# Kernel optimization log

Measured on AMD Instinct MI355X. Metric: run time of the kernel, lower is better.

Reference implementation:

```python
import jax, jax.numpy as jnp
import numpy as np

HEADS = 8
MODEL_DIM = 64
EPS = 1e-5


def _layernorm(x, gamma, beta):
    mu = jnp.mean(x, axis=-1, keepdims=True)
    var = jnp.var(x, axis=-1, keepdims=True)
    return (x - mu) * jax.lax.rsqrt(var + EPS) * gamma + beta


def setup_inputs() -> dict:
    key = jax.random.key(0)
    ks = jax.random.split(key, 5)
    bs, h, w, in_dim = 8, 32, 32, 512
    hd = HEADS * MODEL_DIM  # 512
    s = 0.02
    return {
        "x": jax.random.normal(ks[0], (bs, h, w, in_dim), jnp.float32),
        "Wq": jax.random.normal(ks[1], (in_dim, hd), jnp.float32) * s,
        "Wk": jax.random.normal(ks[2], (in_dim, hd), jnp.float32) * s,
        "Wv": jax.random.normal(ks[3], (in_dim, hd), jnp.float32) * s,
        "Wo": jax.random.normal(ks[4], (hd, in_dim), jnp.float32) * s,
        "gamma": jnp.ones((in_dim,), jnp.float32),
        "beta": jnp.zeros((in_dim,), jnp.float32),
    }


def reference(x, Wq, Wk, Wv, Wo, gamma, beta):
    bs, h, w, in_dim = x.shape
    # pre_norm=True: normalize first; residual uses the normalized x (as in original)
    xn = _layernorm(x, gamma, beta)
    Q = (xn @ Wq).reshape(bs, h, w, HEADS, MODEL_DIM)
    K = (xn @ Wk).reshape(bs, h, w, HEADS, MODEL_DIM)
    V = (xn @ Wv).reshape(bs, h, w, HEADS, MODEL_DIM)
    # full (h,w) x (h,w) correlation per head
    corr = jnp.einsum('bijhd,bklhd->bijhkl', Q, K) / jnp.sqrt(
        jnp.asarray(MODEL_DIM, x.dtype))
    cshape = corr.shape
    attn = jax.nn.softmax(corr.reshape(*cshape[:-2], -1), axis=-1).reshape(cshape)
    logits = jnp.einsum('bijhkl,bklhd->bijhd', attn, V).reshape(bs, h, w, -1)
    out = logits @ Wo + xn
    return out, attn
```

## Files before the change

### kernel.cpp

```cpp
#include <hip/hip_runtime.h>
#include <hip/hip_bf16.h>

typedef __attribute__((ext_vector_type(8))) short bf16x8;
typedef __attribute__((ext_vector_type(4))) short s16x4;
typedef __attribute__((ext_vector_type(4))) float f32x4;

#define DIM 512
#define NH 8
#define HD 64
#define SEQ 1024
#define NB 8
#define ROWS (NB*SEQ)

__device__ __forceinline__ short f2bf(float f) {
  union { float f; unsigned u; } v; v.f = f;
  unsigned r = v.u + 0x7fffu + ((v.u >> 16) & 1u);
  return (short)(r >> 16);
}
__device__ __forceinline__ float bf2f(short s) {
  union { unsigned u; float f; } v; v.u = ((unsigned)(unsigned short)s) << 16;
  return v.f;
}
__device__ __forceinline__ f32x4 mfma16(bf16x8 a, bf16x8 b, f32x4 c) {
  return __builtin_amdgcn_mfma_f32_16x16x32_bf16(a, b, c, 0, 0, 0);
}
__device__ __forceinline__ void gload16(const void* g, void* l) {
  __builtin_amdgcn_global_load_lds(
      (const __attribute__((address_space(1))) unsigned int*)g,
      (__attribute__((address_space(3))) unsigned int*)l, 16, 0, 0);
}
__device__ __forceinline__ void lds_barrier() {
  __builtin_amdgcn_sched_barrier(0);
  asm volatile("s_waitcnt lgkmcnt(0)" ::: "memory");
  __builtin_amdgcn_s_barrier();
  __builtin_amdgcn_sched_barrier(0);
}

__global__ __launch_bounds__(256) void prep_kernel(
    const float* __restrict__ x, const float* __restrict__ gamma,
    const float* __restrict__ beta, short* __restrict__ xnb,
    const float* __restrict__ Wq, const float* __restrict__ Wk,
    const float* __restrict__ Wv, const float* __restrict__ Wo,
    short* __restrict__ WqkvT, short* __restrict__ WoT) {
  __shared__ float tl[64 * 65];
  const int t = threadIdx.x;
  if (blockIdx.x < 2048) {
    const int row = blockIdx.x * 4 + (t >> 6);
    const int lane = t & 63;
    const float4* xr = reinterpret_cast<const float4*>(x + (size_t)row * DIM);
    const float4 a = xr[lane * 2], b2 = xr[lane * 2 + 1];
    float s = a.x + a.y + a.z + a.w + b2.x + b2.y + b2.z + b2.w;
    float sq = a.x*a.x + a.y*a.y + a.z*a.z + a.w*a.w +
               b2.x*b2.x + b2.y*b2.y + b2.z*b2.z + b2.w*b2.w;
    for (int off = 1; off < 64; off <<= 1) {
      s += __shfl_xor(s, off);
      sq += __shfl_xor(sq, off);
    }
    const float mean = s * (1.0f / DIM);
    const float var = sq * (1.0f / DIM) - mean * mean;
    const float rs = rsqrtf(var + 1e-5f);
    const float4 ga = reinterpret_cast<const float4*>(gamma)[lane * 2];
    const float4 gb = reinterpret_cast<const float4*>(gamma)[lane * 2 + 1];
    const float4 ba = reinterpret_cast<const float4*>(beta)[lane * 2];
    const float4 bb = reinterpret_cast<const float4*>(beta)[lane * 2 + 1];
    union { bf16x8 v; short sh[8]; } o;
    o.sh[0] = f2bf((a.x - mean) * rs * ga.x + ba.x);
    o.sh[1] = f2bf((a.y - mean) * rs * ga.y + ba.y);
    o.sh[2] = f2bf((a.z - mean) * rs * ga.z + ba.z);
    o.sh[3] = f2bf((a.w - mean) * rs * ga.w + ba.w);
    o.sh[4] = f2bf((b2.x - mean) * rs * gb.x + bb.x);
    o.sh[5] = f2bf((b2.y - mean) * rs * gb.y + bb.y);
    o.sh[6] = f2bf((b2.z - mean) * rs * gb.z + bb.z);
    o.sh[7] = f2bf((b2.w - mean) * rs * gb.w + bb.w);
    *reinterpret_cast<bf16x8*>(xnb + (size_t)row * DIM + lane * 8) = o.v;
  } else {
    const int bb = blockIdx.x - 2048;
    const int y = bb >> 6;
    const float* W = (y == 0) ? Wq : (y == 1) ? Wk : (y == 2) ? Wv : Wo;
    const int tile = bb & 63;
    const int k0 = (tile >> 3) * 64, n0 = (tile & 7) * 64;
#pragma unroll
    for (int i = 0; i < 16; ++i) {
      const int idx = i * 256 + t;
      const int k = idx >> 6, n = idx & 63;
      tl[n * 65 + k] = W[(size_t)(k0 + k) * 512 + n0 + n];
    }
    __syncthreads();
#pragma unroll
    for (int i = 0; i < 16; ++i) {
      const int idx = i * 256 + t;
      const int n = idx >> 6, k = idx & 63;
      const short v = f2bf(tl[n * 65 + k]);
      if (y < 3) WqkvT[(size_t)(y * 512 + n0 + n) * 512 + k0 + k] = v;
      else       WoT[(size_t)(n0 + n) * 512 + k0 + k] = v;
    }
  }
}

#define GEMM64_MAIN(A_, BT_, m0_, n0_)                                        \
  f32x4 acc[4][4] = {};                                                       \
  {                                                                           \
    const int srow = 8 * w + (lane >> 3);                                     \
    const int sseg = lane & 7;                                                \
    for (int kb = 0; kb < 512; kb += 64) {                                    \
      __syncthreads();                                                        \
      _Pragma("unroll")                                                       \
      for (int p = 0; p < 4; ++p) {                                           \
        const int r = 32 * p + srow;                                          \
        const int gs = 8 * (sseg ^ (r & 7));                                  \
        gload16(A_ + (size_t)(m0_ + r) * 512 + kb + gs,                       \
                &As[(32 * p + 8 * w) * 64]);                                  \
        gload16(BT_ + (size_t)(n0_ + r) * 512 + kb + gs,                      \
                &Bs[(32 * p + 8 * w) * 64]);                                  \
      }                                                                       \
      __syncthreads();                                                        \
      _Pragma("unroll")                                                       \
      for (int half = 0; half < 2; ++half) {                                  \
        bf16x8 af[4], bfr[4];                                                 \
        _Pragma("unroll")                                                     \
        for (int i = 0; i < 4; ++i) {                                         \
          const int ra = 64 * wr + 16 * i + c16;                              \
          af[i] = *reinterpret_cast<const bf16x8*>(                           \
              &As[ra * 64 + 8 * ((4 * half + g) ^ (ra & 7))]);                \
          const int rb = 64 * wc + 16 * i + c16;                              \
          bfr[i] = *reinterpret_cast<const bf16x8*>(                          \
              &Bs[rb * 64 + 8 * ((4 * half + g) ^ (rb & 7))]);                \
        }                                                                     \
        _Pragma("unroll")                                                     \
        for (int i = 0; i < 4; ++i)                                           \
          _Pragma("unroll")                                                   \
          for (int j = 0; j < 4; ++j)                                         \
            acc[i][j] = mfma16(af[i], bfr[j], acc[i][j]);                     \
      }                                                                       \
    }                                                                         \
  }

__global__ __launch_bounds__(256) void gemm_qkv(const short* __restrict__ A,
    const short* __restrict__ BT, short* __restrict__ Qo,
    short* __restrict__ Ko, short* __restrict__ VtF) {
  __shared__ short As[128 * 64];
  __shared__ short Bs[128 * 64];
  const int m0 = blockIdx.x * 128, n0 = blockIdx.y * 128;
  const int t = threadIdx.x, w = t >> 6, lane = t & 63, g = lane >> 4, c16 = lane & 15;
  const int wr = w >> 1, wc = w & 1;
  GEMM64_MAIN(A, BT, m0, n0)
  const int z = n0 >> 9;
  const int nl = n0 & 511;
  if (z < 2) {
    short* O = (z == 0) ? Qo : Ko;
#pragma unroll
    for (int i = 0; i < 4; ++i)
#pragma unroll
      for (int j = 0; j < 4; ++j) {
        const int row0 = m0 + 64 * wr + 16 * i + 4 * g;
        const int col = nl + 64 * wc + 16 * j + c16;
#pragma unroll
        for (int e = 0; e < 4; ++e)
          O[(size_t)(row0 + e) * 512 + col] = f2bf(acc[i][j][e]);
      }
  } else {
#pragma unroll
    for (int i = 0; i < 4; ++i)
#pragma unroll
      for (int j = 0; j < 4; ++j) {
        const int row0 = m0 + 64 * wr + 16 * i + 4 * g;
        const int col = nl + 64 * wc + 16 * j + c16;
        const int bb = row0 >> 10, ss0 = row0 & 1023, hh = col >> 6, dd = col & 63;
        const int cch = ss0 >> 7, kk = ss0 & 127;
        const int w2 = kk >> 5;
        const int g2 = (kk >> 2) & 3;
        const int ee0 = 4 * ((kk >> 4) & 1) + (kk & 3);
        const int dt2 = dd >> 4, c162 = dd & 15;
        s16x4 pv;
#pragma unroll
        for (int e = 0; e < 4; ++e) pv[e] = f2bf(acc[i][j][e]);
        *reinterpret_cast<s16x4*>(
            &VtF[((size_t)((((bb * NH + hh) * 8 + cch) * 4 + w2) * 4 + dt2) << 9) +
                 (g2 * 16 + c162) * 8 + ee0]) = pv;
      }
  }
}

__global__ __launch_bounds__(256) void gemm_out(const short* __restrict__ A,
    const short* __restrict__ BT, const short* __restrict__ xnb,
    float* __restrict__ out) {
  __shared__ short As[128 * 64];
  __shared__ short Bs[128 * 64];
  const int m0 = blockIdx.x * 128, n0 = blockIdx.y * 128;
  const int t = threadIdx.x, w = t >> 6, lane = t & 63, g = lane >> 4, c16 = lane & 15;
  const int wr = w >> 1, wc = w & 1;
  GEMM64_MAIN(A, BT, m0, n0)
#pragma unroll
  for (int i = 0; i < 4; ++i)
#pragma unroll
    for (int j = 0; j < 4; ++j)
#pragma unroll
      for (int e = 0; e < 4; ++e) {
        const int row = m0 + 64 * wr + 16 * i + 4 * g + e;
        const int col = n0 + 64 * wc + 16 * j + c16;
        const size_t idx = (size_t)row * 512 + col;
        out[idx] = acc[i][j][e] + bf2f(xnb[idx]);
      }
}

__global__ __launch_bounds__(256, 2) void attn_kernel(
    const short* __restrict__ Qb, const short* __restrict__ Kb,
    const short* __restrict__ VtF, float* __restrict__ attnOut,
    short* __restrict__ Lg) {
  const int bid = blockIdx.x;
  const int rb = (bid >> 3) & 15;
  const int inst = (bid & 7) * 8 + (bid >> 7);
  const int b = inst >> 3, h = inst & 7;
  const int t = threadIdx.x;
  const int w = t >> 6, lane = t & 63, g = lane >> 4, c16 = lane & 15;
  const int rl = lane >> 3, sgl = lane & 7;
  const int sw = c16 & 7;
  const int rbase = rb * 64;
  const int qrow = t >> 4, qs = t & 15;

  __shared__ __align__(16) char smem[49664];
  __shared__ float red[2][4][16];
  short* Klds = (short*)smem;
  float* P32a = (float*)(smem + 32768);
  float* P32b = (float*)(smem + 41216);

  const short* kgbase = Kb + ((size_t)b * SEQ) * DIM + h * HD;
  const short* vf = VtF + (size_t)inst * 65536;
  const int swz = 8 * (sgl ^ rl);

#define KSTAGE(c_, buf_)                                                       \
  do {                                                                         \
    __builtin_amdgcn_sched_barrier(0);                                         \
    _Pragma("unroll") for (int i_ = 0; i_ < 4; ++i_) {                         \
      gload16(kgbase + (size_t)((c_) * 128 + 32 * w + 8 * i_ + rl) * DIM + swz,\
              &Klds[(buf_) * 8192 + (32 * w + 8 * i_) * 64]);                  \
    }                                                                          \
  } while (0)

  f32x4 acc[16] = {};
  {
    const short* qp = Qb + ((size_t)(b * SEQ + rbase + c16)) * DIM + h * HD + 8 * g;
    const bf16x8 q0 = *reinterpret_cast<const bf16x8*>(qp);
    const bf16x8 q1 = *reinterpret_cast<const bf16x8*>(qp + 32);
    KSTAGE(0, 0);
#pragma unroll
    for (int c = 0; c < 8; ++c) {
      if (c < 7) KSTAGE(c + 1, (c + 1) & 1);
      if (c < 7) { asm volatile("s_waitcnt vmcnt(4)" ::: "memory"); }
      else       { asm volatile("s_waitcnt vmcnt(0)" ::: "memory"); }
      __builtin_amdgcn_sched_barrier(0);
      const short* kl = &Klds[(c & 1) * 8192];
#pragma unroll
      for (int j = 0; j < 2; ++j) {
        const int lr = 32 * w + 16 * j + c16;
        bf16x8 k0 = *reinterpret_cast<const bf16x8*>(&kl[lr * 64 + 8 * (g ^ sw)]);
        bf16x8 k1 = *reinterpret_cast<const bf16x8*>(&kl[lr * 64 + 8 * ((g + 4) ^ sw)]);
        const int tt = c * 2 + j;
        acc[tt] = mfma16(k0, q0, acc[tt]);
        acc[tt] = mfma16(k1, q1, acc[tt]);
      }
    }
  }

  bf16x8 kreg[4], vreg[4];
#pragma unroll
  for (int i = 0; i < 4; ++i)
    kreg[i] = *reinterpret_cast<const bf16x8*>(
        kgbase + (size_t)(32 * w + 8 * i + rl) * DIM + 8 * sgl);
#pragma unroll
  for (int dt = 0; dt < 4; ++dt)
    vreg[dt] = *reinterpret_cast<const bf16x8*>(vf + (size_t)((w * 4 + dt) * 512) + lane * 8);

  bf16x8 pA[8];
  {
    float m = -1e30f;
#pragma unroll
    for (int tt = 0; tt < 16; ++tt)
#pragma unroll
      for (int e = 0; e < 4; ++e) {
        acc[tt][e] *= 0.125f;
        m = fmaxf(m, acc[tt][e]);
      }
    m = fmaxf(m, __shfl_xor(m, 16));
    m = fmaxf(m, __shfl_xor(m, 32));
    if (g == 0) red[0][w][c16] = m;
    lds_barrier();
    m = fmaxf(fmaxf(red[0][0][c16], red[0][1][c16]),
              fmaxf(red[0][2][c16], red[0][3][c16]));
    float sm = 0.f;
#pragma unroll
    for (int tt = 0; tt < 16; ++tt)
#pragma unroll
      for (int e = 0; e < 4; ++e) {
        const float p = __expf(acc[tt][e] - m);
        acc[tt][e] = p;
        sm += p;
      }
    sm += __shfl_xor(sm, 16);
    sm += __shfl_xor(sm, 32);
    if (g == 0) red[1][w][c16] = sm;
    lds_barrier();
    const float rinv = 1.0f / (red[1][0][c16] + red[1][1][c16] +
                               red[1][2][c16] + red[1][3][c16]);
#pragma unroll
    for (int c = 0; c < 8; ++c) {
      union { bf16x8 v; short sh[8]; } u;
#pragma unroll
      for (int j = 0; j < 2; ++j)
#pragma unroll
        for (int e = 0; e < 4; ++e) {
          u.sh[4 * j + e] = f2bf(acc[2 * c + j][e] * rinv);
          acc[2 * c + j][e] = 0.f;
        }
      pA[c] = u.v;
    }
  }

  f32x4 pacc[4] = {};
  f32x4* red2 = reinterpret_cast<f32x4*>(smem + 32768);

#pragma unroll
  for (int tau = 0; tau < 4; ++tau) {
    const bool qk = (tau < 3);
    bf16x8 qn0, qn1;
    if (qk) {
      const short* qn = Qb + ((size_t)(b * SEQ + rbase + (tau + 1) * 16 + c16)) * DIM +
                        h * HD + 8 * g;
      qn0 = *reinterpret_cast<const bf16x8*>(qn);
      qn1 = *reinterpret_cast<const bf16x8*>(qn + 32);
    }
    float* astore = attnOut + (size_t)b * 8388608 +
                    (size_t)(rbase + tau * 16 + qrow) * 8192 + h * 1024;
#pragma unroll
    for (int c = 0; c < 8; ++c) {
      lds_barrier();
      if (qk) {
#pragma unroll
        for (int i = 0; i < 4; ++i)
          *reinterpret_cast<bf16x8*>(
              &Klds[(c & 1) * 8192 + (32 * w + 8 * i + rl) * 64 + 8 * (sgl ^ rl)]) = kreg[i];
      }
      {
        float* P32w = (c & 1) ? P32b : P32a;
        union { bf16x8 v; short sh[8]; } u; u.v = pA[c];
        f32x4 v0, v1;
#pragma unroll
        for (int e = 0; e < 4; ++e) { v0[e] = bf2f(u.sh[e]); v1[e] = bf2f(u.sh[4 + e]); }
        *reinterpret_cast<f32x4*>(&P32w[c16 * 132 + 32 * w + 4 * g]) = v0;
        *reinterpret_cast<f32x4*>(&P32w[c16 * 132 + 32 * w + 16 + 4 * g]) = v1;
      }
      if (qk) {
#pragma unroll
        for (int i = 0; i < 4; ++i)
          kreg[i] = *reinterpret_cast<const bf16x8*>(
              kgbase + (size_t)((((c + 1) & 7)) * 128 + 32 * w + 8 * i + rl) * DIM + 8 * sgl);
      }
      lds_barrier();
      {
        const float* P32r = (c & 1) ? P32b : P32a;
        const f32x4 s0 = *reinterpret_cast<const f32x4*>(&P32r[qrow * 132 + 4 * qs]);
        const f32x4 s1 = *reinterpret_cast<const f32x4*>(&P32r[qrow * 132 + 64 + 4 * qs]);
        __builtin_nontemporal_store(s0, reinterpret_cast<f32x4*>(astore + c * 128 + 4 * qs));
        __builtin_nontemporal_store(s1, reinterpret_cast<f32x4*>(astore + c * 128 + 64 + 4 * qs));
      }
      if (qk) {
        const short* kl = &Klds[(c & 1) * 8192];
#pragma unroll
        for (int j = 0; j < 2; ++j) {
          const int lr = 32 * w + 16 * j + c16;
          bf16x8 k0 = *reinterpret_cast<const bf16x8*>(&kl[lr * 64 + 8 * (g ^ sw)]);
          bf16x8 k1 = *reinterpret_cast<const bf16x8*>(&kl[lr * 64 + 8 * ((g + 4) ^ sw)]);
          const int tt = c * 2 + j;
          acc[tt] = mfma16(k0, qn0, acc[tt]);
          acc[tt] = mfma16(k1, qn1, acc[tt]);
        }
      }
#pragma unroll
      for (int dt = 0; dt < 4; ++dt)
        pacc[dt] = mfma16(pA[c], vreg[dt], pacc[dt]);
      if (!(tau == 3 && c == 7)) {
#pragma unroll
        for (int dt = 0; dt < 4; ++dt)
          vreg[dt] = *reinterpret_cast<const bf16x8*>(
              vf + (size_t)(((((c + 1) & 7) * 4 + w) * 4 + dt) * 512) + lane * 8);
      }
    }

    if (qk) {
      float m = -1e30f;
#pragma unroll
      for (int tt = 0; tt < 16; ++tt)
#pragma unroll
        for (int e = 0; e < 4; ++e) {
          acc[tt][e] *= 0.125f;
          m = fmaxf(m, acc[tt][e]);
        }
      m = fmaxf(m, __shfl_xor(m, 16));
      m = fmaxf(m, __shfl_xor(m, 32));
      if (g == 0) red[0][w][c16] = m;
      lds_barrier();
#pragma unroll
      for (int dt = 0; dt < 4; ++dt) red2[(w * 4 + dt) * 64 + lane] = pacc[dt];
#pragma unroll
      for (int dt = 0; dt < 4; ++dt)
#pragma unroll
        for (int e = 0; e < 4; ++e) pacc[dt][e] = 0.f;
      m = fmaxf(fmaxf(red[0][0][c16], red[0][1][c16]),
                fmaxf(red[0][2][c16], red[0][3][c16]));
      float sm = 0.f;
#pragma unroll
      for (int tt = 0; tt < 16; ++tt)
#pragma unroll
        for (int e = 0; e < 4; ++e) {
          const float pe = __expf(acc[tt][e] - m);
          acc[tt][e] = pe;
          sm += pe;
        }
      sm += __shfl_xor(sm, 16);
      sm += __shfl_xor(sm, 32);
      if (g == 0) red[1][w][c16] = sm;
      lds_barrier();
      {
        const int dt = w;
        f32x4 s = red2[dt * 64 + lane];
#pragma unroll
        for (int w2 = 1; w2 < 4; ++w2) {
          f32x4 o = red2[(w2 * 4 + dt) * 64 + lane];
#pragma unroll
          for (int e = 0; e < 4; ++e) s[e] += o[e];
        }
        short* lrow = Lg + ((size_t)(b * SEQ + rbase + tau * 16 + 4 * g)) * DIM +
                      h * HD + 16 * dt + c16;
#pragma unroll
        for (int e = 0; e < 4; ++e) lrow[(size_t)e * DIM] = f2bf(s[e]);
      }
      const float rinv = 1.0f / (red[1][0][c16] + red[1][1][c16] +
                                 red[1][2][c16] + red[1][3][c16]);
#pragma unroll
      for (int c = 0; c < 8; ++c) {
        union { bf16x8 v; short sh[8]; } u;
#pragma unroll
        for (int j = 0; j < 2; ++j)
#pragma unroll
          for (int e = 0; e < 4; ++e) {
            u.sh[4 * j + e] = f2bf(acc[2 * c + j][e] * rinv);
            acc[2 * c + j][e] = 0.f;
          }
        pA[c] = u.v;
      }
    } else {
      lds_barrier();
#pragma unroll
      for (int dt = 0; dt < 4; ++dt) red2[(w * 4 + dt) * 64 + lane] = pacc[dt];
      lds_barrier();
      const int dt = w;
      f32x4 s = red2[dt * 64 + lane];
#pragma unroll
      for (int w2 = 1; w2 < 4; ++w2) {
        f32x4 o = red2[(w2 * 4 + dt) * 64 + lane];
#pragma unroll
        for (int e = 0; e < 4; ++e) s[e] += o[e];
      }
      short* lrow = Lg + ((size_t)(b * SEQ + rbase + 48 + 4 * g)) * DIM +
                    h * HD + 16 * dt + c16;
#pragma unroll
      for (int e = 0; e < 4; ++e) lrow[(size_t)e * DIM] = f2bf(s[e]);
    }
  }
}

extern "C" void kernel_launch(void* const* d_in, const int* in_sizes, int n_in,
                              void* d_out, int out_size, void* d_ws, size_t ws_size,
                              hipStream_t stream) {
  const float* x = (const float*)d_in[0];
  const float* Wq = (const float*)d_in[1];
  const float* Wk = (const float*)d_in[2];
  const float* Wv = (const float*)d_in[3];
  const float* Wo = (const float*)d_in[4];
  const float* gamma = (const float*)d_in[5];
  const float* beta = (const float*)d_in[6];
  float* out = (float*)d_out;
  float* attn = out + (size_t)ROWS * DIM;

  char* ws = (char*)d_ws;
  short* xnb = (short*)ws;
  short* WqkvT = (short*)(ws + (size_t)8 * 1024 * 1024);
  short* WoT = WqkvT + 1536 * 512;
  short* Qb = (short*)(ws + (size_t)10 * 1024 * 1024);
  short* Kbp = (short*)(ws + (size_t)18 * 1024 * 1024);
  short* VtF = (short*)(ws + (size_t)26 * 1024 * 1024);
  short* Lg = (short*)(ws + (size_t)34 * 1024 * 1024);

  prep_kernel<<<2304, 256, 0, stream>>>(x, gamma, beta, xnb, Wq, Wk, Wv, Wo, WqkvT, WoT);
  gemm_qkv<<<dim3(64, 12), 256, 0, stream>>>(xnb, WqkvT, Qb, Kbp, VtF);
  attn_kernel<<<1024, 256, 0, stream>>>(Qb, Kbp, VtF, attn, Lg);
  gemm_out<<<dim3(64, 4), 256, 0, stream>>>(Lg, WoT, xnb, out);
}
```

Measured before the change: 144.1 us.

## Shrink attention kernel LDS footprint with a swizzled single P buffer and aliased reductions

Replaces the two padded fp32 probability staging buffers with one unpadded buffer that uses an XOR swizzle to avoid bank conflicts. The softmax max/sum reduction arrays are aliased into that buffer, and the PV partial-sum reduction scratch moves onto the K tile region. This cuts static shared memory from about 50 KB to 40 KB so more workgroups can be resident per CU. The cost is an extra barrier in the per-tile softmax path and tighter reuse of LDS regions, which raises the risk of ordering hazards.

```diff
diff --git a/kernel.cpp b/kernel.cpp
--- a/kernel.cpp
+++ b/kernel.cpp
@@ -215,14 +215,16 @@
   const int w = t >> 6, lane = t & 63, g = lane >> 4, c16 = lane & 15;
   const int rl = lane >> 3, sgl = lane & 7;
   const int sw = c16 & 7;
+  const int sw32 = 4 * (c16 & 7);
   const int rbase = rb * 64;
   const int qrow = t >> 4, qs = t & 15;
-
-  __shared__ __align__(16) char smem[49664];
-  __shared__ float red[2][4][16];
+  const int rsw = 4 * (qrow & 7);
+
+  __shared__ __align__(16) char smem[40960];
   short* Klds = (short*)smem;
-  float* P32a = (float*)(smem + 32768);
-  float* P32b = (float*)(smem + 41216);
+  float* P32 = (float*)(smem + 32768);
+  float* redm = P32;
+  float* reds = P32 + 64;
 
   const short* kgbase = Kb + ((size_t)b * SEQ) * DIM + h * HD;
   const short* vf = VtF + (size_t)inst * 65536;
@@ -283,10 +285,10 @@
       }
     m = fmaxf(m, __shfl_xor(m, 16));
     m = fmaxf(m, __shfl_xor(m, 32));
-    if (g == 0) red[0][w][c16] = m;
+    if (g == 0) redm[w * 16 + c16] = m;
     lds_barrier();
-    m = fmaxf(fmaxf(red[0][0][c16], red[0][1][c16]),
-              fmaxf(red[0][2][c16], red[0][3][c16]));
+    m = fmaxf(fmaxf(redm[c16], redm[16 + c16]),
+              fmaxf(redm[32 + c16], redm[48 + c16]));
     float sm = 0.f;
 #pragma unroll
     for (int tt = 0; tt < 16; ++tt)
@@ -298,10 +300,10 @@
       }
     sm += __shfl_xor(sm, 16);
     sm += __shfl_xor(sm, 32);
-    if (g == 0) red[1][w][c16] = sm;
+    if (g == 0) reds[w * 16 + c16] = sm;
     lds_barrier();
-    const float rinv = 1.0f / (red[1][0][c16] + red[1][1][c16] +
-                               red[1][2][c16] + red[1][3][c16]);
+    const float rinv = 1.0f / (reds[c16] + reds[16 + c16] +
+                               reds[32 + c16] + reds[48 + c16]);
 #pragma unroll
     for (int c = 0; c < 8; ++c) {
       union { bf16x8 v; short sh[8]; } u;
@@ -317,7 +319,7 @@
   }
 
   f32x4 pacc[4] = {};
-  f32x4* red2 = reinterpret_cast<f32x4*>(smem + 32768);
+  f32x4* red2 = reinterpret_cast<f32x4*>(smem);
 
 #pragma unroll
   for (int tau = 0; tau < 4; ++tau) {
@@ -341,13 +343,12 @@
               &Klds[(c & 1) * 8192 + (32 * w + 8 * i + rl) * 64 + 8 * (sgl ^ rl)]) = kreg[i];
       }
       {
-        float* P32w = (c & 1) ? P32b : P32a;
         union { bf16x8 v; short sh[8]; } u; u.v = pA[c];
         f32x4 v0, v1;
 #pragma unroll
         for (int e = 0; e < 4; ++e) { v0[e] = bf2f(u.sh[e]); v1[e] = bf2f(u.sh[4 + e]); }
-        *reinterpret_cast<f32x4*>(&P32w[c16 * 132 + 32 * w + 4 * g]) = v0;
-        *reinterpret_cast<f32x4*>(&P32w[c16 * 132 + 32 * w + 16 + 4 * g]) = v1;
+        *reinterpret_cast<f32x4*>(&P32[c16 * 128 + ((32 * w + 4 * g) ^ sw32)]) = v0;
+        *reinterpret_cast<f32x4*>(&P32[c16 * 128 + ((32 * w + 16 + 4 * g) ^ sw32)]) = v1;
       }
       if (qk) {
 #pragma unroll
@@ -357,9 +358,8 @@
       }
       lds_barrier();
       {
-        const float* P32r = (c & 1) ? P32b : P32a;
-        const f32x4 s0 = *reinterpret_cast<const f32x4*>(&P32r[qrow * 132 + 4 * qs]);
-        const f32x4 s1 = *reinterpret_cast<const f32x4*>(&P32r[qrow * 132 + 64 + 4 * qs]);
+        const f32x4 s0 = *reinterpret_cast<const f32x4*>(&P32[qrow * 128 + ((4 * qs) ^ rsw)]);
+        const f32x4 s1 = *reinterpret_cast<const f32x4*>(&P32[qrow * 128 + ((64 + 4 * qs) ^ rsw)]);
         __builtin_nontemporal_store(s0, reinterpret_cast<f32x4*>(astore + c * 128 + 4 * qs));
         __builtin_nontemporal_store(s1, reinterpret_cast<f32x4*>(astore + c * 128 + 64 + 4 * qs));
       }
@@ -397,16 +397,17 @@
         }
       m = fmaxf(m, __shfl_xor(m, 16));
       m = fmaxf(m, __shfl_xor(m, 32));
-      if (g == 0) red[0][w][c16] = m;
-      lds_barrier();
+      lds_barrier();
+      if (g == 0) redm[w * 16 + c16] = m;
 #pragma unroll
       for (int dt = 0; dt < 4; ++dt) red2[(w * 4 + dt) * 64 + lane] = pacc[dt];
 #pragma unroll
       for (int dt = 0; dt < 4; ++dt)
 #pragma unroll
         for (int e = 0; e < 4; ++e) pacc[dt][e] = 0.f;
-      m = fmaxf(fmaxf(red[0][0][c16], red[0][1][c16]),
-                fmaxf(red[0][2][c16], red[0][3][c16]));
+      lds_barrier();
+      m = fmaxf(fmaxf(redm[c16], redm[16 + c16]),
+                fmaxf(redm[32 + c16], redm[48 + c16]));
       float sm = 0.f;
 #pragma unroll
       for (int tt = 0; tt < 16; ++tt)
@@ -418,8 +419,7 @@
         }
       sm += __shfl_xor(sm, 16);
       sm += __shfl_xor(sm, 32);
-      if (g == 0) red[1][w][c16] = sm;
-      lds_barrier();
+      if (g == 0) reds[w * 16 + c16] = sm;
       {
         const int dt = w;
         f32x4 s = red2[dt * 64 + lane];
@@ -434,8 +434,9 @@
 #pragma unroll
         for (int e = 0; e < 4; ++e) lrow[(size_t)e * DIM] = f2bf(s[e]);
       }
-      const float rinv = 1.0f / (red[1][0][c16] + red[1][1][c16] +
-                                 red[1][2][c16] + red[1][3][c16]);
+      lds_barrier();
+      const float rinv = 1.0f / (reds[c16] + reds[16 + c16] +
+                                 reds[32 + c16] + reds[48 + c16]);
 #pragma unroll
       for (int c = 0; c < 8; ++c) {
         union { bf16x8 v; short sh[8]; } u;
```

After: 142.9 us. No clear change (-0.8%).
